# Kernel tuning notes

Measured on AMD Instinct MI355X. Metric: run time of the kernel, lower is better.

The kernel has to match this reference:

```python
import jax, jax.numpy as jnp
import numpy as np
from jax import lax

ANCHOR_SCALES = (8, 16, 32)
ANCHOR_RATIOS = (0.5, 1.0, 2.0)
A = 9
BASE_SIZE = 32
FEATURE_STRIDE = 16
PRE_NMS = 1000
POST_NMS = 300
NMS_THRESH = 0.7
MIN_SIZE = 16.0
BN_EPS = 1e-5

IN_DIM = 256
BASE_OUT = 256
N, FH, FW = 4, 80, 80
IMG_H = IMG_W = FH * FEATURE_STRIDE


def generate_anchors():
    w = h = float(BASE_SIZE)
    cx = 0.5 * (w - 1.0); cy = 0.5 * (h - 1.0)
    size = w * h
    out = []
    for r in ANCHOR_RATIOS:
        ws = np.round(np.sqrt(size / r)); hs = np.round(ws * r)
        for s in ANCHOR_SCALES:
            W = ws * s; H = hs * s
            out.append([cx - 0.5 * (W - 1), cy - 0.5 * (H - 1), cx + 0.5 * (W - 1), cy + 0.5 * (H - 1)])
    return np.array(out, np.float32)


def splash_anchors(fH, fW):
    base = generate_anchors()  # (A,4)
    sx = np.arange(fW, dtype=np.float32) * FEATURE_STRIDE
    sy = np.arange(fH, dtype=np.float32) * FEATURE_STRIDE
    yy, xx = np.meshgrid(sy, sx, indexing='ij')
    shifts = np.stack([xx.ravel(), yy.ravel(), xx.ravel(), yy.ravel()], 1)  # (H*W,4), row-major over (y,x)
    return jnp.asarray((base[None] + shifts[:, None]).reshape(-1, 4))  # (H*W*A,4)


def conv2d(x, w, pad):
    return lax.conv_general_dilated(x, w, (1, 1), [(pad, pad), (pad, pad)],
                                    dimension_numbers=('NCHW', 'OIHW', 'NCHW'))


def bn(x, g, b, m, v):
    inv = g / jnp.sqrt(v + BN_EPS)
    return x * inv[None, :, None, None] + (b - m * inv)[None, :, None, None]


def mish(x):
    return x * jnp.tanh(jax.nn.softplus(x))


def decode_clip(anchors, deltas, img_h, img_w):
    aw = anchors[:, 2] - anchors[:, 0] + 1.0
    ah = anchors[:, 3] - anchors[:, 1] + 1.0
    acx = anchors[:, 0] + 0.5 * aw; acy = anchors[:, 1] + 0.5 * ah
    pcx = deltas[:, 0] * aw + acx; pcy = deltas[:, 1] * ah + acy
    pw = jnp.exp(deltas[:, 2]) * aw; ph = jnp.exp(deltas[:, 3]) * ah
    x1 = jnp.clip(pcx - 0.5 * pw, 0.0, img_w - 1.0)
    y1 = jnp.clip(pcy - 0.5 * ph, 0.0, img_h - 1.0)
    x2 = jnp.clip(pcx + 0.5 * pw, 0.0, img_w - 1.0)
    y2 = jnp.clip(pcy + 0.5 * ph, 0.0, img_h - 1.0)
    return jnp.stack([x1, y1, x2, y2], 1)


def iou_matrix(b):
    area = (b[:, 2] - b[:, 0] + 1.0) * (b[:, 3] - b[:, 1] + 1.0)
    x1 = jnp.maximum(b[:, None, 0], b[None, :, 0])
    y1 = jnp.maximum(b[:, None, 1], b[None, :, 1])
    x2 = jnp.minimum(b[:, None, 2], b[None, :, 2])
    y2 = jnp.minimum(b[:, None, 3], b[None, :, 3])
    inter = jnp.clip(x2 - x1 + 1.0, 0.0) * jnp.clip(y2 - y1 + 1.0, 0.0)
    return inter / (area[:, None] + area[None, :] - inter)


def proposal_one(scores, deltas, anchors, img_h, img_w):
    boxes = decode_clip(anchors, deltas, img_h, img_w)
    ws = boxes[:, 2] - boxes[:, 0] + 1.0
    hs = boxes[:, 3] - boxes[:, 1] + 1.0
    s = jnp.where((ws >= MIN_SIZE) & (hs >= MIN_SIZE), scores, -1e9)
    _, top = lax.top_k(s, PRE_NMS)
    b = boxes[top]  # (PRE_NMS,4) sorted by fg score desc
    iou = iou_matrix(b)
    rng = jnp.arange(PRE_NMS)
    def body(i, supp):
        alive = jnp.logical_not(supp[i])
        return supp | (alive & (iou[i] > NMS_THRESH) & (rng > i))
    supp = lax.fori_loop(0, PRE_NMS, body, jnp.zeros(PRE_NMS, bool))
    keep = jnp.logical_not(supp)
    order = jnp.argsort(jnp.logical_not(keep))  # stable: kept first, in score order
    sel = order[:POST_NMS]
    return b[sel] * keep[sel][:, None]  # zero-pad rows past the last kept box


def rpn_forward(x, conv_w, conv_b, bn1_g, bn1_b, bn1_m, bn1_v,
                cls_w, bn2_g, bn2_b, bn2_m, bn2_v,
                reg_w, bn3_g, bn3_b, bn3_m, bn3_v, img_h, img_w):
    n, _, fH, fW = x.shape
    base = bn(mish(conv2d(x, conv_w, 1) + conv_b[None, :, None, None]), bn1_g, bn1_b, bn1_m, bn1_v)
    rpn_reg = bn(conv2d(base, reg_w, 0), bn3_g, bn3_b, bn3_m, bn3_v)
    rpn_reg = rpn_reg.transpose(0, 2, 3, 1).reshape(n, -1, 4)  # (n, H*W*A, 4)
    score = bn(conv2d(base, cls_w, 0), bn2_g, bn2_b, bn2_m, bn2_v).transpose(0, 2, 3, 1)
    fg = jax.nn.softmax(score.reshape(n, fH, fW, A, 2), axis=4)[..., 1].reshape(n, -1)
    anchors = splash_anchors(fH, fW)
    ih, iw = float(img_h), float(img_w)
    rois = jax.vmap(lambda s, d: proposal_one(s, d, anchors, ih, iw))(fg, rpn_reg)
    return fg, rpn_reg, rois


def setup_inputs():
    key = jax.random.key(0)
    ks = jax.random.split(key, 16)
    return {
        'x': jax.random.normal(ks[0], (N, IN_DIM, FH, FW), jnp.float32),
        'conv_w': jax.random.normal(ks[1], (BASE_OUT, IN_DIM, 3, 3), jnp.float32) * 0.02,
        'conv_b': jnp.zeros((BASE_OUT,), jnp.float32),
        'bn1_g': jax.random.normal(ks[2], (BASE_OUT,)) * 0.1 + 1.0,
        'bn1_b': jax.random.normal(ks[3], (BASE_OUT,)) * 0.1,
        'bn1_m': jax.random.normal(ks[4], (BASE_OUT,)) * 0.1,
        'bn1_v': jax.random.uniform(ks[5], (BASE_OUT,)) + 0.5,
        'cls_w': jax.random.normal(ks[6], (2 * A, BASE_OUT, 1, 1)) * 0.05,
        'bn2_g': jax.random.normal(ks[7], (2 * A,)) * 0.1 + 1.0,
        'bn2_b': jax.random.normal(ks[8], (2 * A,)) * 0.1,
        'bn2_m': jax.random.normal(ks[9], (2 * A,)) * 0.1,
        'bn2_v': jax.random.uniform(ks[10], (2 * A,)) + 0.5,
        'reg_w': jax.random.normal(ks[11], (4 * A, BASE_OUT, 1, 1)) * 0.05,
        'bn3_g': jax.random.normal(ks[12], (4 * A,)) * 0.1 + 1.0,
        'bn3_b': jax.random.normal(ks[13], (4 * A,)) * 0.1,
        'bn3_m': jax.random.normal(ks[14], (4 * A,)) * 0.1,
        'bn3_v': jax.random.uniform(ks[15], (4 * A,)) + 0.5,
        'img_h': IMG_H,
        'img_w': IMG_W,
    }


def reference(x, conv_w, conv_b, bn1_g, bn1_b, bn1_m, bn1_v,
              cls_w, bn2_g, bn2_b, bn2_m, bn2_v,
              reg_w, bn3_g, bn3_b, bn3_m, bn3_v, img_h, img_w):
    return rpn_forward(x, conv_w, conv_b, bn1_g, bn1_b, bn1_m, bn1_v,
                       cls_w, bn2_g, bn2_b, bn2_m, bn2_v,
                       reg_w, bn3_g, bn3_b, bn3_m, bn3_v, img_h, img_w)
```

## Files before the change

### kernel.cpp

```cpp
#include <hip/hip_runtime.h>
#include <stdint.h>

typedef unsigned int u32;
typedef unsigned long long u64;
typedef _Float16 f16;
typedef __attribute__((ext_vector_type(8))) _Float16 f16x8;
typedef __attribute__((ext_vector_type(4))) float f32x4;

#define NB 4
#define CIN 256
#define HW 80
#define PX (HW*HW)
#define NA 9
#define NANCH (PX*NA)
#define PRE 1000
#define POST 300
#define CANDN 4096

#define O_REG  (NB*NANCH)
#define O_ROIS (O_REG + NB*NANCH*4)

#define WS_WPREP 0ull
#define WS_BASE  2949120ull
#define WS_BOX   29163520ull
#define WS_KEY   32849920ull
#define WS_GH    33771520ull
#define WS_TBOX  35868672ull
#define WS_MASK  35932672ull

__constant__ float c_aw[9] = {360.f,720.f,1440.f,256.f,512.f,1024.f,184.f,368.f,736.f};
__constant__ float c_ah[9] = {176.f,352.f,704.f,256.f,512.f,1024.f,368.f,736.f,1472.f};

__global__ void k_prepw(const float* __restrict__ w, f16* __restrict__ Wp)
{
    int id = blockIdx.x*256 + threadIdx.x;
    if (id >= 9*8*256) return;
    int co = id & 255;
    int tc = id >> 8;
    int t = tc >> 3, cib = tc & 7;
    __align__(16) f16 hb[40];
    __align__(16) f16 mb[40];
    #pragma unroll
    for (int k = 32; k < 40; ++k) { hb[k] = (f16)0.f; mb[k] = (f16)0.f; }
    #pragma unroll
    for (int ci = 0; ci < 32; ++ci) {
        float wv = w[((size_t)co*256 + (cib*32 + ci))*9 + t];
        f16 h = (f16)wv;
        f16 m = (f16)((wv - (float)h) * 4096.f);
        hb[ci] = h; mb[ci] = m;
    }
    f16* oh = Wp + (size_t)tc*20480 + (size_t)co*40;
    f16* om = oh + 10240;
    #pragma unroll
    for (int k = 0; k < 5; ++k) {
        *(f16x8*)(oh + k*8) = *(const f16x8*)(hb + k*8);
        *(f16x8*)(om + k*8) = *(const f16x8*)(mb + k*8);
    }
}

__launch_bounds__(256, 2)
__global__ void k_conv3(const float* __restrict__ x, const f16* __restrict__ Wp,
                        const float* __restrict__ cbias,
                        const float* __restrict__ g1, const float* __restrict__ b1,
                        const float* __restrict__ m1, const float* __restrict__ v1,
                        float* __restrict__ base)
{
    __shared__ __align__(16) f16 ldsA[10240];
    __shared__ __align__(16) f16 ldsX[14400];
    int tid = threadIdx.x;
    int lane = tid & 63, wid = tid >> 6;
    int q = lane >> 4, l16 = lane & 15;
    int wc = (wid >> 1) * 64, wr = (wid & 1) * 4;
    int bid = blockIdx.x;
    int cb = bid & 1, pxb = bid >> 1;
    int n = pxb / 50, rem = pxb % 50;
    int h0 = (rem / 5) * 8, w0 = (rem % 5) * 16;

    f32x4 acch[4][4], accl[4][4];
    #pragma unroll
    for (int i = 0; i < 4; ++i)
        #pragma unroll
        for (int j = 0; j < 4; ++j) {
            acch[i][j] = (f32x4){0.f,0.f,0.f,0.f};
            accl[i][j] = (f32x4){0.f,0.f,0.f,0.f};
        }

    const float* xn = x + (size_t)n*CIN*PX;

    for (int cb8 = 0; cb8 < 8; ++cb8) {
        int ci0 = cb8 * 32;
        for (int t = 0; t < 9; ++t) {
            __syncthreads();
            if (t == 0) {
                for (int task = tid; task < 320; task += 256) {
                    int r = task >> 5, ci = task & 31;
                    int hh = h0 - 1 + r;
                    bool rowok = (hh >= 0) && (hh < HW);
                    const float* src = xn + (size_t)(ci0 + ci)*PX + hh*HW + (w0 - 1);
                    f16* dh = ldsX + r*18*40 + ci;
                    f16* dm = dh + 7200;
                    #pragma unroll
                    for (int cc = 0; cc < 18; ++cc) {
                        int ww = w0 - 1 + cc;
                        float v = (rowok && ww >= 0 && ww < HW) ? src[cc] : 0.f;
                        f16 h = (f16)v;
                        f16 m = (f16)((v - (float)h) * 4096.f);
                        dh[cc*40] = h;
                        dm[cc*40] = m;
                    }
                }
            }
            {
                const f16* wsrc = Wp + (size_t)(t*8 + cb8)*20480;
                #pragma unroll
                for (int c = 0; c < 5; ++c) {
                    int idx = c*256 + tid;
                    int part = idx / 640, off = idx - part*640;
                    *(f16x8*)(ldsA + (size_t)idx*8) =
                        *(const f16x8*)(wsrc + part*10240 + cb*5120 + off*8);
                }
            }
            __syncthreads();

            int dh_ = t / 3, dw_ = t - dh_*3;
            f16x8 Ah[4], Am[4];
            #pragma unroll
            for (int i = 0; i < 4; ++i) {
                int e = (wc + i*16 + l16)*40 + q*8;
                Ah[i] = *(const f16x8*)(ldsA + e);
                Am[i] = *(const f16x8*)(ldsA + 5120 + e);
            }
            #pragma unroll
            for (int j = 0; j < 4; ++j) {
                int pos = (wr + j + dh_)*18 + l16 + dw_;
                int e = pos*40 + q*8;
                f16x8 Bh = *(const f16x8*)(ldsX + e);
                f16x8 Bm = *(const f16x8*)(ldsX + 7200 + e);
                #pragma unroll
                for (int i = 0; i < 4; ++i) {
                    acch[i][j] = __builtin_amdgcn_mfma_f32_16x16x32_f16(Ah[i], Bh, acch[i][j], 0, 0, 0);
                    accl[i][j] = __builtin_amdgcn_mfma_f32_16x16x32_f16(Ah[i], Bm, accl[i][j], 0, 0, 0);
                    accl[i][j] = __builtin_amdgcn_mfma_f32_16x16x32_f16(Am[i], Bh, accl[i][j], 0, 0, 0);
                }
            }
        }
    }
    #pragma unroll
    for (int i = 0; i < 4; ++i) {
        #pragma unroll
        for (int rg = 0; rg < 4; ++rg) {
            int co = cb*128 + wc + i*16 + q*4 + rg;
            float cbv = cbias[co];
            float inv = g1[co] / sqrtf(v1[co] + 1e-5f);
            float ad  = b1[co] - m1[co]*inv;
            #pragma unroll
            for (int j = 0; j < 4; ++j) {
                float tval = acch[i][j][rg] + accl[i][j][rg]*(1.f/4096.f) + cbv;
                float sp = fmaxf(tval, 0.f) + log1pf(expf(-fabsf(tval)));
                float mi = tval * tanhf(sp);
                int h = h0 + wr + j, w = w0 + l16;
                base[(size_t)(n*CIN + co)*PX + h*HW + w] = mi*inv + ad;
            }
        }
    }
}

__launch_bounds__(256)
__global__ void k_heads(const float* __restrict__ base,
                        const float* __restrict__ clsw, const float* __restrict__ regw,
                        const float* __restrict__ g2, const float* __restrict__ b2,
                        const float* __restrict__ m2, const float* __restrict__ v2,
                        const float* __restrict__ g3, const float* __restrict__ b3,
                        const float* __restrict__ m3, const float* __restrict__ v3,
                        float* __restrict__ out)
{
    __shared__ float wt[256*56];
    int tid = threadIdx.x;
    for (int i = tid; i < 54*256; i += 256) {
        int co = i >> 8, ci = i & 255;
        float v = (co < 18) ? clsw[i] : regw[i - 18*256];
        wt[ci*56 + co] = v;
    }
    __syncthreads();
    int gp = blockIdx.x*256 + tid;
    int n = gp / PX, p = gp % PX;
    float acc[54];
    #pragma unroll
    for (int i = 0; i < 54; ++i) acc[i] = 0.f;
    const float* bp = base + (size_t)n*CIN*PX + p;
    for (int ci = 0; ci < 256; ++ci) {
        float xv = bp[(size_t)ci*PX];
        const float* wr = &wt[ci*56];
        #pragma unroll
        for (int co = 0; co < 54; ++co) acc[co] = fmaf(wr[co], xv, acc[co]);
    }
    int fgb = n*NANCH + p*NA;
    #pragma unroll
    for (int a = 0; a < NA; ++a) {
        float i0 = g2[2*a]   / sqrtf(v2[2*a]   + 1e-5f);
        float i1 = g2[2*a+1] / sqrtf(v2[2*a+1] + 1e-5f);
        float s0 = acc[2*a]*i0   + (b2[2*a]   - m2[2*a]*i0);
        float s1 = acc[2*a+1]*i1 + (b2[2*a+1] - m2[2*a+1]*i1);
        float mx = fmaxf(s0, s1);
        float e0 = expf(s0 - mx), e1 = expf(s1 - mx);
        out[fgb + a] = e1 / (e0 + e1);
    }
    size_t rb = (size_t)O_REG + (size_t)n*NANCH*4 + (size_t)p*36;
    #pragma unroll
    for (int c = 0; c < 36; ++c) {
        float iv = g3[c] / sqrtf(v3[c] + 1e-5f);
        out[rb + c] = acc[18 + c]*iv + (b3[c] - m3[c]*iv);
    }
}

__global__ void k_decode(const float* __restrict__ out,
                         float* __restrict__ boxes, u32* __restrict__ keys)
{
    int gi = blockIdx.x*256 + threadIdx.x;
    int n = gi / NANCH, i = gi % NANCH;
    int a = i % NA, p = i / NA;
    int wx = p % HW, hy = p / HW;
    const float4 d = *(const float4*)&out[O_REG + (size_t)n*NANCH*4 + (size_t)i*4];
    float aw = c_aw[a], ah = c_ah[a];
    float acx = 16.f + 16.f*(float)wx;
    float acy = 16.f + 16.f*(float)hy;
    float pcx = d.x*aw + acx;
    float pcy = d.y*ah + acy;
    float pw = expf(d.z)*aw;
    float ph = expf(d.w)*ah;
    float x1 = fminf(fmaxf(pcx - 0.5f*pw, 0.f), 1279.f);
    float y1 = fminf(fmaxf(pcy - 0.5f*ph, 0.f), 1279.f);
    float x2 = fminf(fmaxf(pcx + 0.5f*pw, 0.f), 1279.f);
    float y2 = fminf(fmaxf(pcy + 0.5f*ph, 0.f), 1279.f);
    float wsz = x2 - x1 + 1.f, hsz = y2 - y1 + 1.f;
    float sc = out[(size_t)n*NANCH + i];
    float s = (wsz >= 16.f && hsz >= 16.f) ? sc : -1e9f;
    *(float4*)&boxes[((size_t)n*NANCH + i)*4] = make_float4(x1, y1, x2, y2);
    u32 u = __float_as_uint(s);
    u = (u & 0x80000000u) ? ~u : (u | 0x80000000u);
    keys[(size_t)n*NANCH + i] = u;
}

__launch_bounds__(256)
__global__ void k_hist(const u32* __restrict__ keys, u32* __restrict__ ghp)
{
    __shared__ u32 hh[4096];
    int bid = blockIdx.x;
    int n = bid >> 6, slice = bid & 63;
    int tid = threadIdx.x;
    #pragma unroll
    for (int k = 0; k < 16; ++k) hh[tid + k*256] = 0;
    __syncthreads();
    const u32* kp = keys + (size_t)n*NANCH + slice*900;
    for (int i = tid; i < 900; i += 256)
        atomicAdd(&hh[kp[i] >> 20], 1u);
    __syncthreads();
    u32* gp = ghp + ((size_t)n*64 + slice)*2048;
    #pragma unroll
    for (int k = 0; k < 8; ++k) {
        int j = tid + k*256;
        gp[j] = (hh[2*j] & 0xFFFFu) | (hh[2*j+1] << 16);
    }
}

__launch_bounds__(1024)
__global__ void k_select(const u32* __restrict__ keys, const u32* __restrict__ ghp,
                         const float* __restrict__ boxes, float* __restrict__ topbox)
{
    __shared__ u32 h1[4096];
    __shared__ u32 h2[4][4096];
    __shared__ u32 ss[1025];
    __shared__ int sB1, sA1, sB2, scnt;
    __shared__ u64 cand[CANDN];
    int n = blockIdx.x, tid = threadIdx.x, wid = tid >> 6;

    const u32* gp = ghp + (size_t)n*64*2048;
    u32 c0=0,c1=0,c2=0,c3=0;
    for (int s = 0; s < 64; ++s) {
        const u32* w = gp + s*2048 + 2*tid;
        u32 a = w[0], b = w[1];
        c0 += a & 0xFFFFu; c1 += a >> 16; c2 += b & 0xFFFFu; c3 += b >> 16;
    }
    h1[4*tid+0]=c0; h1[4*tid+1]=c1; h1[4*tid+2]=c2; h1[4*tid+3]=c3;
    ss[tid] = c0+c1+c2+c3;
    if (tid == 0) scnt = 0;
    __syncthreads();
    for (int off = 1; off < 1024; off <<= 1) {
        u32 v = (tid + off < 1024) ? ss[tid + off] : 0u;
        __syncthreads();
        ss[tid] += v;
        __syncthreads();
    }
    {
        u32 nxt = (tid == 1023) ? 0u : ss[tid + 1];
        if (ss[tid] >= PRE && nxt < PRE) {
            u32 c = nxt;
            for (int b = 4*tid+3; b >= 4*tid; --b) {
                c += h1[b];
                if (c >= PRE) { sB1 = b; sA1 = (int)(c - h1[b]); break; }
            }
        }
    }
    __syncthreads();
    int B1 = sB1, A1 = sA1;
    for (int k = tid; k < 4*4096; k += 1024) ((u32*)h2)[k] = 0;
    __syncthreads();

    const u32* kp = keys + (size_t)n*NANCH;
    for (int i = tid; i < NANCH; i += 1024) {
        u32 k = kp[i];
        int top = (int)(k >> 20);
        if (top > B1) {
            int pos = atomicAdd(&scnt, 1);
            if (pos < CANDN) cand[pos] = ~(((u64)k << 32) | (u64)(0xFFFFFFFFu - (u32)i));
        } else if (top == B1) {
            atomicAdd(&h2[wid & 3][(k >> 8) & 0xFFFu], 1u);
        }
    }
    __syncthreads();
    {
        int b = 4*tid;
        u32 d0 = h2[0][b]+h2[1][b]+h2[2][b]+h2[3][b];
        u32 d1 = h2[0][b+1]+h2[1][b+1]+h2[2][b+1]+h2[3][b+1];
        u32 d2 = h2[0][b+2]+h2[1][b+2]+h2[2][b+2]+h2[3][b+2];
        u32 d3 = h2[0][b+3]+h2[1][b+3]+h2[2][b+3]+h2[3][b+3];
        ss[tid] = d0+d1+d2+d3;
    }
    __syncthreads();
    for (int off = 1; off < 1024; off <<= 1) {
        u32 v = (tid + off < 1024) ? ss[tid + off] : 0u;
        __syncthreads();
        ss[tid] += v;
        __syncthreads();
    }
    {
        u32 nxt = (tid == 1023) ? 0u : ss[tid + 1];
        if ((u32)A1 + ss[tid] >= PRE && (u32)A1 + nxt < PRE) {
            u32 c = (u32)A1 + nxt;
            for (int b = 4*tid+3; b >= 4*tid; --b) {
                u32 hv = h2[0][b]+h2[1][b]+h2[2][b]+h2[3][b];
                c += hv;
                if (c >= PRE) { sB2 = b; break; }
            }
        }
    }
    __syncthreads();
    int B2 = sB2;

    for (int i = tid; i < NANCH; i += 1024) {
        u32 k = kp[i];
        if ((int)(k >> 20) == B1 && (int)((k >> 8) & 0xFFFu) >= B2) {
            int pos = atomicAdd(&scnt, 1);
            if (pos < CANDN) cand[pos] = ~(((u64)k << 32) | (u64)(0xFFFFFFFFu - (u32)i));
        }
    }
    __syncthreads();
    int cnt = min(scnt, CANDN);
    int N = (cnt <= 2048) ? 2048 : CANDN;
    for (int i = cnt + tid; i < N; i += 1024) cand[i] = ~0ull;
    __syncthreads();
    for (int k = 2; k <= N; k <<= 1) {
        for (int j = k >> 1; j > 0; j >>= 1) {
            for (int t = tid; t < N/2; t += 1024) {
                int i1 = 2*t - (t & (j - 1));
                int i2 = i1 + j;
                u64 va = cand[i1], vb = cand[i2];
                bool up = ((i1 & k) == 0);
                if ((va > vb) == up) { cand[i1] = vb; cand[i2] = va; }
            }
            __syncthreads();
        }
    }
    for (int r = tid; r < PRE; r += 1024) {
        u64 c = ~cand[r];
        u32 idx = 0xFFFFFFFFu - (u32)(c & 0xFFFFFFFFull);
        *(float4*)&topbox[((size_t)n*PRE + r)*4] =
            *(const float4*)&boxes[((size_t)n*NANCH + idx)*4];
    }
}

__launch_bounds__(256)
__global__ void k_iou(const float* __restrict__ topbox, u64* __restrict__ masks)
{
    int n = blockIdx.x >> 4, chunk = blockIdx.x & 15;
    __shared__ float4 bs[PRE];
    for (int i = threadIdx.x; i < PRE; i += 256)
        bs[i] = *(const float4*)&topbox[((size_t)n*PRE + i)*4];
    __syncthreads();
    int il = threadIdx.x >> 2;
    int wq = threadIdx.x & 3;
    int i = chunk*64 + il;
    if (i >= PRE) return;
    float4 bi = bs[i];
    float ai = (bi.z - bi.x + 1.f) * (bi.w - bi.y + 1.f);
    u64* mrow = masks + ((size_t)n*PRE + i)*16;
    for (int w = wq*4; w < wq*4 + 4; ++w) {
        u64 m = 0;
        int jn = min(64, PRE - w*64);
        for (int jj = 0; jj < jn; ++jj) {
            int j = w*64 + jj;
            float4 bj = bs[j];
            float xx1 = fmaxf(bi.x, bj.x);
            float yy1 = fmaxf(bi.y, bj.y);
            float xx2 = fminf(bi.z, bj.z);
            float yy2 = fminf(bi.w, bj.w);
            float iw = fmaxf(xx2 - xx1 + 1.f, 0.f);
            float ih = fmaxf(yy2 - yy1 + 1.f, 0.f);
            float inter = iw * ih;
            float aj = (bj.z - bj.x + 1.f) * (bj.w - bj.y + 1.f);
            float iou = inter / (ai + aj - inter);
            if ((j > i) && (iou > 0.7f)) m |= (1ull << jj);
        }
        mrow[w] = m;
    }
}

__launch_bounds__(64)
__global__ void k_nms(const u64* __restrict__ masks, const float* __restrict__ topbox,
                      float* __restrict__ out)
{
    int n = blockIdx.x;
    int lane = threadIdx.x;
    int w = lane & 15;
    const u64* M = masks + (size_t)n*PRE*16;
    u64 remv = 0, keep = 0;
    u64 m0 = M[0*16+w], m1 = M[1*16+w], m2 = M[2*16+w], m3 = M[3*16+w];
    u64 m4 = M[4*16+w], m5 = M[5*16+w], m6 = M[6*16+w], m7 = M[7*16+w];
#define PROC(MR, II) { \
    int ii = (II); \
    u64 rw = __shfl(remv, ii >> 6, 64); \
    if (((rw >> (ii & 63)) & 1ull) == 0ull) { \
        remv |= MR; \
        if (w == (ii >> 6)) keep |= (1ull << (ii & 63)); \
    } }
    for (int b = 0; b < PRE; b += 8) {
        PROC(m0, b+0); m0 = (b+8  < PRE) ? M[(size_t)(b+8)*16 + w]  : 0ull;
        PROC(m1, b+1); m1 = (b+9  < PRE) ? M[(size_t)(b+9)*16 + w]  : 0ull;
        PROC(m2, b+2); m2 = (b+10 < PRE) ? M[(size_t)(b+10)*16 + w] : 0ull;
        PROC(m3, b+3); m3 = (b+11 < PRE) ? M[(size_t)(b+11)*16 + w] : 0ull;
        PROC(m4, b+4); m4 = (b+12 < PRE) ? M[(size_t)(b+12)*16 + w] : 0ull;
        PROC(m5, b+5); m5 = (b+13 < PRE) ? M[(size_t)(b+13)*16 + w] : 0ull;
        PROC(m6, b+6); m6 = (b+14 < PRE) ? M[(size_t)(b+14)*16 + w] : 0ull;
        PROC(m7, b+7); m7 = (b+15 < PRE) ? M[(size_t)(b+15)*16 + w] : 0ull;
    }
#undef PROC
    __shared__ int cnts[16];
    __shared__ int pfx[17];
    __shared__ u32 list[PRE];
    if (lane < 16) cnts[lane] = __popcll(keep);
    __syncthreads();
    if (lane == 0) {
        int s = 0;
        for (int t = 0; t < 16; ++t) { pfx[t] = s; s += cnts[t]; }
        pfx[16] = s;
    }
    __syncthreads();
    if (lane < 16) {
        int pos = pfx[lane];
        u64 kk = keep;
        for (int b = 0; b < 64; ++b)
            if ((kk >> b) & 1ull) list[pos++] = (u32)(lane*64 + b);
    }
    __syncthreads();
    int total = pfx[16];
    for (int k = lane; k < POST; k += 64) {
        float4 v = make_float4(0.f, 0.f, 0.f, 0.f);
        if (k < total) {
            u32 r = list[k];
            v = *(const float4*)&topbox[((size_t)n*PRE + r)*4];
        }
        *(float4*)&out[O_ROIS + ((size_t)n*POST + k)*4] = v;
    }
}

extern "C" void kernel_launch(void* const* d_in, const int* in_sizes, int n_in,
                              void* d_out, int out_size, void* d_ws, size_t ws_size,
                              hipStream_t stream)
{
    const float* x      = (const float*)d_in[0];
    const float* conv_w = (const float*)d_in[1];
    const float* conv_b = (const float*)d_in[2];
    const float* g1 = (const float*)d_in[3];
    const float* b1 = (const float*)d_in[4];
    const float* m1 = (const float*)d_in[5];
    const float* v1 = (const float*)d_in[6];
    const float* clsw = (const float*)d_in[7];
    const float* g2 = (const float*)d_in[8];
    const float* b2 = (const float*)d_in[9];
    const float* m2 = (const float*)d_in[10];
    const float* v2 = (const float*)d_in[11];
    const float* regw = (const float*)d_in[12];
    const float* g3 = (const float*)d_in[13];
    const float* b3 = (const float*)d_in[14];
    const float* m3 = (const float*)d_in[15];
    const float* v3 = (const float*)d_in[16];

    char* ws = (char*)d_ws;
    f16*   Wp     = (f16*)(ws + WS_WPREP);
    float* base   = (float*)(ws + WS_BASE);
    float* boxes  = (float*)(ws + WS_BOX);
    u32*   keys   = (u32*)(ws + WS_KEY);
    u32*   ghp    = (u32*)(ws + WS_GH);
    float* topbox = (float*)(ws + WS_TBOX);
    u64*   masks  = (u64*)(ws + WS_MASK);
    float* out = (float*)d_out;

    k_prepw<<<72, 256, 0, stream>>>(conv_w, Wp);
    k_conv3<<<400, 256, 0, stream>>>(x, Wp, conv_b, g1, b1, m1, v1, base);
    k_heads<<<100, 256, 0, stream>>>(base, clsw, regw, g2, b2, m2, v2, g3, b3, m3, v3, out);
    k_decode<<<900, 256, 0, stream>>>(out, boxes, keys);
    k_hist<<<256, 256, 0, stream>>>(keys, ghp);
    k_select<<<4, 1024, 0, stream>>>(keys, ghp, boxes, topbox);
    k_iou<<<64, 256, 0, stream>>>(topbox, masks);
    k_nms<<<4, 64, 0, stream>>>(masks, topbox, out);
}
```

Measured before the change: 465.8 us.

## Split conv3 output channels finer, fuse decode/hist into heads, widen IoU grid

The 3x3 conv now splits output channels into four 64-wide blocks instead of two 128-wide ones. That doubles the grid to 800 blocks, halves the per-block weight tile and accumulators, raises occupancy to three blocks per CU, and adds a blockIdx swizzle. Box decoding, key generation and the score histogram are folded into the heads kernel, which removes two launches and a round trip through global memory. The IoU kernel gives each thread a single 64-bit mask word across 252 blocks to get more parallelism. The conv change re-stages the input tile once per channel block, so input LDS staging work doubles.

```diff
diff --git a/kernel.cpp b/kernel.cpp
--- a/kernel.cpp
+++ b/kernel.cpp
@@ -58,27 +58,27 @@
     }
 }
 
-__launch_bounds__(256, 2)
+__launch_bounds__(256, 3)
 __global__ void k_conv3(const float* __restrict__ x, const f16* __restrict__ Wp,
                         const float* __restrict__ cbias,
                         const float* __restrict__ g1, const float* __restrict__ b1,
                         const float* __restrict__ m1, const float* __restrict__ v1,
                         float* __restrict__ base)
 {
-    __shared__ __align__(16) f16 ldsA[10240];
+    __shared__ __align__(16) f16 ldsA[5120];
     __shared__ __align__(16) f16 ldsX[14400];
     int tid = threadIdx.x;
     int lane = tid & 63, wid = tid >> 6;
     int q = lane >> 4, l16 = lane & 15;
-    int wc = (wid >> 1) * 64, wr = (wid & 1) * 4;
-    int bid = blockIdx.x;
-    int cb = bid & 1, pxb = bid >> 1;
+    int wc = (wid >> 1) * 32, wr = (wid & 1) * 4;
+    int virt = (blockIdx.x & 7)*100 + (blockIdx.x >> 3);
+    int cb = virt & 3, pxb = virt >> 2;
     int n = pxb / 50, rem = pxb % 50;
     int h0 = (rem / 5) * 8, w0 = (rem % 5) * 16;
 
-    f32x4 acch[4][4], accl[4][4];
-    #pragma unroll
-    for (int i = 0; i < 4; ++i)
+    f32x4 acch[2][4], accl[2][4];
+    #pragma unroll
+    for (int i = 0; i < 2; ++i)
         #pragma unroll
         for (int j = 0; j < 4; ++j) {
             acch[i][j] = (f32x4){0.f,0.f,0.f,0.f};
@@ -113,22 +113,24 @@
             {
                 const f16* wsrc = Wp + (size_t)(t*8 + cb8)*20480;
                 #pragma unroll
-                for (int c = 0; c < 5; ++c) {
+                for (int c = 0; c < 3; ++c) {
                     int idx = c*256 + tid;
-                    int part = idx / 640, off = idx - part*640;
-                    *(f16x8*)(ldsA + (size_t)idx*8) =
-                        *(const f16x8*)(wsrc + part*10240 + cb*5120 + off*8);
+                    if (idx < 640) {
+                        int part = idx / 320, off = idx - part*320;
+                        *(f16x8*)(ldsA + (size_t)idx*8) =
+                            *(const f16x8*)(wsrc + part*10240 + cb*2560 + off*8);
+                    }
                 }
             }
             __syncthreads();
 
             int dh_ = t / 3, dw_ = t - dh_*3;
-            f16x8 Ah[4], Am[4];
+            f16x8 Ah[2], Am[2];
             #pragma unroll
-            for (int i = 0; i < 4; ++i) {
+            for (int i = 0; i < 2; ++i) {
                 int e = (wc + i*16 + l16)*40 + q*8;
                 Ah[i] = *(const f16x8*)(ldsA + e);
-                Am[i] = *(const f16x8*)(ldsA + 5120 + e);
+                Am[i] = *(const f16x8*)(ldsA + 2560 + e);
             }
             #pragma unroll
             for (int j = 0; j < 4; ++j) {
@@ -137,7 +139,7 @@
                 f16x8 Bh = *(const f16x8*)(ldsX + e);
                 f16x8 Bm = *(const f16x8*)(ldsX + 7200 + e);
                 #pragma unroll
-                for (int i = 0; i < 4; ++i) {
+                for (int i = 0; i < 2; ++i) {
                     acch[i][j] = __builtin_amdgcn_mfma_f32_16x16x32_f16(Ah[i], Bh, acch[i][j], 0, 0, 0);
                     accl[i][j] = __builtin_amdgcn_mfma_f32_16x16x32_f16(Ah[i], Bm, accl[i][j], 0, 0, 0);
                     accl[i][j] = __builtin_amdgcn_mfma_f32_16x16x32_f16(Am[i], Bh, accl[i][j], 0, 0, 0);
@@ -146,10 +148,10 @@
         }
     }
     #pragma unroll
-    for (int i = 0; i < 4; ++i) {
+    for (int i = 0; i < 2; ++i) {
         #pragma unroll
         for (int rg = 0; rg < 4; ++rg) {
-            int co = cb*128 + wc + i*16 + q*4 + rg;
+            int co = cb*64 + wc + i*16 + q*4 + rg;
             float cbv = cbias[co];
             float inv = g1[co] / sqrtf(v1[co] + 1e-5f);
             float ad  = b1[co] - m1[co]*inv;
@@ -172,15 +174,19 @@
                         const float* __restrict__ m2, const float* __restrict__ v2,
                         const float* __restrict__ g3, const float* __restrict__ b3,
                         const float* __restrict__ m3, const float* __restrict__ v3,
-                        float* __restrict__ out)
+                        float* __restrict__ out, float* __restrict__ boxes,
+                        u32* __restrict__ keys, u32* __restrict__ ghp)
 {
     __shared__ float wt[256*56];
+    __shared__ u32 hh[4096];
     int tid = threadIdx.x;
     for (int i = tid; i < 54*256; i += 256) {
         int co = i >> 8, ci = i & 255;
         float v = (co < 18) ? clsw[i] : regw[i - 18*256];
         wt[ci*56 + co] = v;
     }
+    #pragma unroll
+    for (int k = 0; k < 16; ++k) hh[tid + k*256] = 0;
     __syncthreads();
     int gp = blockIdx.x*256 + tid;
     int n = gp / PX, p = gp % PX;
@@ -194,6 +200,7 @@
         #pragma unroll
         for (int co = 0; co < 54; ++co) acc[co] = fmaf(wr[co], xv, acc[co]);
     }
+    float fgv[9];
     int fgb = n*NANCH + p*NA;
     #pragma unroll
     for (int a = 0; a < NA; ++a) {
@@ -203,63 +210,46 @@
         float s1 = acc[2*a+1]*i1 + (b2[2*a+1] - m2[2*a+1]*i1);
         float mx = fmaxf(s0, s1);
         float e0 = expf(s0 - mx), e1 = expf(s1 - mx);
-        out[fgb + a] = e1 / (e0 + e1);
-    }
+        fgv[a] = e1 / (e0 + e1);
+        out[fgb + a] = fgv[a];
+    }
+    float regv[36];
     size_t rb = (size_t)O_REG + (size_t)n*NANCH*4 + (size_t)p*36;
     #pragma unroll
     for (int c = 0; c < 36; ++c) {
         float iv = g3[c] / sqrtf(v3[c] + 1e-5f);
-        out[rb + c] = acc[18 + c]*iv + (b3[c] - m3[c]*iv);
-    }
-}
-
-__global__ void k_decode(const float* __restrict__ out,
-                         float* __restrict__ boxes, u32* __restrict__ keys)
-{
-    int gi = blockIdx.x*256 + threadIdx.x;
-    int n = gi / NANCH, i = gi % NANCH;
-    int a = i % NA, p = i / NA;
+        regv[c] = acc[18 + c]*iv + (b3[c] - m3[c]*iv);
+        out[rb + c] = regv[c];
+    }
     int wx = p % HW, hy = p / HW;
-    const float4 d = *(const float4*)&out[O_REG + (size_t)n*NANCH*4 + (size_t)i*4];
-    float aw = c_aw[a], ah = c_ah[a];
     float acx = 16.f + 16.f*(float)wx;
     float acy = 16.f + 16.f*(float)hy;
-    float pcx = d.x*aw + acx;
-    float pcy = d.y*ah + acy;
-    float pw = expf(d.z)*aw;
-    float ph = expf(d.w)*ah;
-    float x1 = fminf(fmaxf(pcx - 0.5f*pw, 0.f), 1279.f);
-    float y1 = fminf(fmaxf(pcy - 0.5f*ph, 0.f), 1279.f);
-    float x2 = fminf(fmaxf(pcx + 0.5f*pw, 0.f), 1279.f);
-    float y2 = fminf(fmaxf(pcy + 0.5f*ph, 0.f), 1279.f);
-    float wsz = x2 - x1 + 1.f, hsz = y2 - y1 + 1.f;
-    float sc = out[(size_t)n*NANCH + i];
-    float s = (wsz >= 16.f && hsz >= 16.f) ? sc : -1e9f;
-    *(float4*)&boxes[((size_t)n*NANCH + i)*4] = make_float4(x1, y1, x2, y2);
-    u32 u = __float_as_uint(s);
-    u = (u & 0x80000000u) ? ~u : (u | 0x80000000u);
-    keys[(size_t)n*NANCH + i] = u;
-}
-
-__launch_bounds__(256)
-__global__ void k_hist(const u32* __restrict__ keys, u32* __restrict__ ghp)
-{
-    __shared__ u32 hh[4096];
-    int bid = blockIdx.x;
-    int n = bid >> 6, slice = bid & 63;
-    int tid = threadIdx.x;
-    #pragma unroll
-    for (int k = 0; k < 16; ++k) hh[tid + k*256] = 0;
-    __syncthreads();
-    const u32* kp = keys + (size_t)n*NANCH + slice*900;
-    for (int i = tid; i < 900; i += 256)
-        atomicAdd(&hh[kp[i] >> 20], 1u);
-    __syncthreads();
-    u32* gp = ghp + ((size_t)n*64 + slice)*2048;
+    #pragma unroll
+    for (int a = 0; a < NA; ++a) {
+        float aw = c_aw[a], ah = c_ah[a];
+        float pcx = regv[4*a+0]*aw + acx;
+        float pcy = regv[4*a+1]*ah + acy;
+        float pw = expf(regv[4*a+2])*aw;
+        float ph = expf(regv[4*a+3])*ah;
+        float x1 = fminf(fmaxf(pcx - 0.5f*pw, 0.f), 1279.f);
+        float y1 = fminf(fmaxf(pcy - 0.5f*ph, 0.f), 1279.f);
+        float x2 = fminf(fmaxf(pcx + 0.5f*pw, 0.f), 1279.f);
+        float y2 = fminf(fmaxf(pcy + 0.5f*ph, 0.f), 1279.f);
+        float wsz = x2 - x1 + 1.f, hsz = y2 - y1 + 1.f;
+        float s = (wsz >= 16.f && hsz >= 16.f) ? fgv[a] : -1e9f;
+        int i = p*NA + a;
+        *(float4*)&boxes[((size_t)n*NANCH + i)*4] = make_float4(x1, y1, x2, y2);
+        u32 u = __float_as_uint(s);
+        u = (u & 0x80000000u) ? ~u : (u | 0x80000000u);
+        keys[(size_t)n*NANCH + i] = u;
+        atomicAdd(&hh[u >> 20], 1u);
+    }
+    __syncthreads();
+    u32* gp2 = ghp + ((size_t)n*25 + (blockIdx.x % 25))*2048;
     #pragma unroll
     for (int k = 0; k < 8; ++k) {
         int j = tid + k*256;
-        gp[j] = (hh[2*j] & 0xFFFFu) | (hh[2*j+1] << 16);
+        gp2[j] = (hh[2*j] & 0xFFFFu) | (hh[2*j+1] << 16);
     }
 }
 
@@ -274,9 +264,9 @@
     __shared__ u64 cand[CANDN];
     int n = blockIdx.x, tid = threadIdx.x, wid = tid >> 6;
 
-    const u32* gp = ghp + (size_t)n*64*2048;
+    const u32* gp = ghp + (size_t)n*25*2048;
     u32 c0=0,c1=0,c2=0,c3=0;
-    for (int s = 0; s < 64; ++s) {
+    for (int s = 0; s < 25; ++s) {
         const u32* w = gp + s*2048 + 2*tid;
         u32 a = w[0], b = w[1];
         c0 += a & 0xFFFFu; c1 += a >> 16; c2 += b & 0xFFFFu; c3 += b >> 16;
@@ -382,37 +372,33 @@
 __launch_bounds__(256)
 __global__ void k_iou(const float* __restrict__ topbox, u64* __restrict__ masks)
 {
-    int n = blockIdx.x >> 4, chunk = blockIdx.x & 15;
+    int n = blockIdx.x / 63, chunk = blockIdx.x % 63;
     __shared__ float4 bs[PRE];
     for (int i = threadIdx.x; i < PRE; i += 256)
         bs[i] = *(const float4*)&topbox[((size_t)n*PRE + i)*4];
     __syncthreads();
-    int il = threadIdx.x >> 2;
-    int wq = threadIdx.x & 3;
-    int i = chunk*64 + il;
+    int i = chunk*16 + (threadIdx.x >> 4);
+    int w = threadIdx.x & 15;
     if (i >= PRE) return;
     float4 bi = bs[i];
     float ai = (bi.z - bi.x + 1.f) * (bi.w - bi.y + 1.f);
-    u64* mrow = masks + ((size_t)n*PRE + i)*16;
-    for (int w = wq*4; w < wq*4 + 4; ++w) {
-        u64 m = 0;
-        int jn = min(64, PRE - w*64);
-        for (int jj = 0; jj < jn; ++jj) {
-            int j = w*64 + jj;
-            float4 bj = bs[j];
-            float xx1 = fmaxf(bi.x, bj.x);
-            float yy1 = fmaxf(bi.y, bj.y);
-            float xx2 = fminf(bi.z, bj.z);
-            float yy2 = fminf(bi.w, bj.w);
-            float iw = fmaxf(xx2 - xx1 + 1.f, 0.f);
-            float ih = fmaxf(yy2 - yy1 + 1.f, 0.f);
-            float inter = iw * ih;
-            float aj = (bj.z - bj.x + 1.f) * (bj.w - bj.y + 1.f);
-            float iou = inter / (ai + aj - inter);
-            if ((j > i) && (iou > 0.7f)) m |= (1ull << jj);
-        }
-        mrow[w] = m;
-    }
+    u64 m = 0;
+    int jn = min(64, PRE - w*64);
+    for (int jj = 0; jj < jn; ++jj) {
+        int j = w*64 + jj;
+        float4 bj = bs[j];
+        float xx1 = fmaxf(bi.x, bj.x);
+        float yy1 = fmaxf(bi.y, bj.y);
+        float xx2 = fminf(bi.z, bj.z);
+        float yy2 = fminf(bi.w, bj.w);
+        float iw = fmaxf(xx2 - xx1 + 1.f, 0.f);
+        float ih = fmaxf(yy2 - yy1 + 1.f, 0.f);
+        float inter = iw * ih;
+        float aj = (bj.z - bj.x + 1.f) * (bj.w - bj.y + 1.f);
+        float iou = inter / (ai + aj - inter);
+        if ((j > i) && (iou > 0.7f)) m |= (1ull << jj);
+    }
+    masks[((size_t)n*PRE + i)*16 + w] = m;
 }
 
 __launch_bounds__(64)
@@ -506,11 +492,10 @@
     float* out = (float*)d_out;
 
     k_prepw<<<72, 256, 0, stream>>>(conv_w, Wp);
-    k_conv3<<<400, 256, 0, stream>>>(x, Wp, conv_b, g1, b1, m1, v1, base);
-    k_heads<<<100, 256, 0, stream>>>(base, clsw, regw, g2, b2, m2, v2, g3, b3, m3, v3, out);
-    k_decode<<<900, 256, 0, stream>>>(out, boxes, keys);
-    k_hist<<<256, 256, 0, stream>>>(keys, ghp);
+    k_conv3<<<800, 256, 0, stream>>>(x, Wp, conv_b, g1, b1, m1, v1, base);
+    k_heads<<<100, 256, 0, stream>>>(base, clsw, regw, g2, b2, m2, v2, g3, b3, m3, v3,
+                                     out, boxes, keys, ghp);
     k_select<<<4, 1024, 0, stream>>>(keys, ghp, boxes, topbox);
-    k_iou<<<64, 256, 0, stream>>>(topbox, masks);
+    k_iou<<<252, 256, 0, stream>>>(topbox, masks);
     k_nms<<<4, 64, 0, stream>>>(masks, topbox, out);
 }
```

New measurement: 455.7 us. 2.2% less time.
